# Kernel tuning notes

Measured on AMD Instinct MI355X. Metric: run time of the kernel, lower is better.

## Reference

```python
import jax, jax.numpy as jnp
import numpy as np

WINDOW_SIZE = 11
SIGMA = 1.5
WEIGHTS = np.array([0.0448, 0.2856, 0.3001, 0.2363, 0.1333], dtype=np.float32)
LEVELS = 5


def _gaussian(ws, sigma):
    x = np.arange(ws, dtype=np.float32)
    g = np.exp(-((x - ws // 2) ** 2) / (2.0 * sigma ** 2))
    return g / g.sum()


def _window3d(ws, channel):
    g = _gaussian(ws, SIGMA)
    w3 = np.einsum('i,j,k->ijk', g, g, g).astype(np.float32)  # [ws,ws,ws]
    # OIDHW, depthwise: O=channel, I=1
    return jnp.asarray(np.broadcast_to(w3[None, None], (channel, 1, ws, ws, ws)))


def _conv3d(x, w, channel):
    return jax.lax.conv_general_dilated(
        x, w, window_strides=(1, 1, 1), padding='VALID',
        dimension_numbers=('NCDHW', 'OIDHW', 'NCDHW'),
        feature_group_count=channel)


def _avg_pool3d(x):
    s = jax.lax.reduce_window(x, 0.0, jax.lax.add,
                              (1, 1, 2, 2, 2), (1, 1, 2, 2, 2), 'VALID')
    return s / 8.0


def _ssim(img1, img2, window_size):
    _, channel, d, h, w = img1.shape
    # val_range=None branch: L derived from img1 statistics
    max_val = jnp.where(jnp.max(img1) > 128, 255.0, 1.0)
    min_val = jnp.where(jnp.min(img1) < -0.5, -1.0, 0.0)
    L = max_val - min_val
    real_size = min(window_size, d, h, w)
    win = _window3d(real_size, channel)

    mu1 = _conv3d(img1, win, channel)
    mu2 = _conv3d(img2, win, channel)
    mu1_sq = mu1 * mu1
    mu2_sq = mu2 * mu2
    mu1_mu2 = mu1 * mu2
    sigma1_sq = _conv3d(img1 * img1, win, channel) - mu1_sq
    sigma2_sq = _conv3d(img2 * img2, win, channel) - mu2_sq
    sigma12 = _conv3d(img1 * img2, win, channel) - mu1_mu2

    C1 = (0.01 * L) ** 2
    C2 = (0.03 * L) ** 2
    v1 = 2.0 * sigma12 + C2
    v2 = sigma1_sq + sigma2_sq + C2
    cs = jnp.mean(v1 / v2)
    ssim_map = (2.0 * mu1_mu2 + C1) * v1 / ((mu1_sq + mu2_sq + C1) * v2)
    return jnp.mean(ssim_map), cs


def setup_inputs() -> dict:
    key = jax.random.key(0)
    k1, k2 = jax.random.split(key)
    shape = (2, 1, 192, 192, 192)
    img1 = jax.random.normal(k1, shape, dtype=jnp.float32)
    img2 = jax.random.normal(k2, shape, dtype=jnp.float32)
    return {"img1": img1, "img2": img2}


def reference(img1, img2):
    weights = jnp.asarray(WEIGHTS)
    ssims, mcs = [], []
    for _ in range(LEVELS):
        sim, cs = _ssim(img1, img2, WINDOW_SIZE)
        ssims.append(sim)
        mcs.append(cs)
        img1 = _avg_pool3d(img1)
        img2 = _avg_pool3d(img2)
    ssims = jnp.stack(ssims)
    mcs = jnp.stack(mcs)
    pow1 = mcs ** weights
    pow2 = ssims ** weights
    return jnp.prod(pow1[:-1]) * pow2[-1]
```

## Files before the change

kernel.cpp:

```cpp
#include <hip/hip_runtime.h>
#include <math.h>


__device__ __forceinline__ unsigned enc_f(float f) {
    unsigned u = __float_as_uint(f);
    return (u & 0x80000000u) ? ~u : (u | 0x80000000u);
}
__device__ __forceinline__ float dec_f(unsigned e) {
    unsigned u = (e & 0x80000000u) ? (e ^ 0x80000000u) : ~e;
    return __uint_as_float(u);
}

__global__ void init_kernel(float* wsf) {
    unsigned* wsu = (unsigned*)wsf;
    int t = threadIdx.x;
    if (t < 10)       wsf[t] = 0.0f;
    else if (t < 15)  wsu[t] = 0xFFFFFFFFu;
    else if (t < 20)  wsu[t] = 0u;
    else if (t == 20) wsu[t] = 0u;
}

struct PyrParams {
    const float* src[2];
    float* dst[2][4];
};

__launch_bounds__(256, 4)
__global__ void pyramid_kernel(PyrParams P, float* wsf) {
    __shared__ float L1[16 * 256];
    __shared__ float L2[512];
    __shared__ float L3[64];
    __shared__ float smn[4], smx[4];
    unsigned* wsu = (unsigned*)wsf;

    const int tid = threadIdx.x;
    int blk = blockIdx.x;
    int r = blk % 216; blk /= 216;
    int batch = blk & 1;
    int im = blk >> 1;
    const int rx = r % 6, ry = (r / 6) % 6, rz = r / 36;

    const long N0 = 192L * 192 * 192;
    const float* src = P.src[im] + (long)batch * N0;
    float* d1 = P.dst[im][0] + (long)batch * 96 * 96 * 96;
    float* d2 = P.dst[im][1] + (long)batch * 48 * 48 * 48;
    float* d3 = P.dst[im][2] + (long)batch * 24 * 24 * 24;
    float* d4 = P.dst[im][3] + (long)batch * 12 * 12 * 12;

    const int tx = tid & 15, ty = tid >> 4;
    float mnv[5], mxv[5];
#pragma unroll
    for (int l = 0; l < 5; l++) { mnv[l] = INFINITY; mxv[l] = -INFINITY; }

    const long D = 192, D2 = 192L * 192;
    const int gx = 2 * (rx * 16 + tx);
    const int gy = 2 * (ry * 16 + ty);
#pragma unroll 4
    for (int z = 0; z < 16; z++) {
        const int gz = 2 * (rz * 16 + z);
        long base = (long)gz * D2 + (long)gy * D + gx;
        float2 a00 = *(const float2*)(src + base);
        float2 a01 = *(const float2*)(src + base + D);
        float2 a10 = *(const float2*)(src + base + D2);
        float2 a11 = *(const float2*)(src + base + D2 + D);
        float lo = fminf(fminf(fminf(a00.x, a00.y), fminf(a01.x, a01.y)),
                         fminf(fminf(a10.x, a10.y), fminf(a11.x, a11.y)));
        float hi = fmaxf(fmaxf(fmaxf(a00.x, a00.y), fmaxf(a01.x, a01.y)),
                         fmaxf(fmaxf(a10.x, a10.y), fmaxf(a11.x, a11.y)));
        mnv[0] = fminf(mnv[0], lo); mxv[0] = fmaxf(mxv[0], hi);
        float s = (a00.x + a00.y + a01.x + a01.y +
                   a10.x + a10.y + a11.x + a11.y) * 0.125f;
        mnv[1] = fminf(mnv[1], s); mxv[1] = fmaxf(mxv[1], s);
        d1[(long)(rz * 16 + z) * 96 * 96 + (ry * 16 + ty) * 96 + (rx * 16 + tx)] = s;
        L1[z * 256 + ty * 16 + tx] = s;
    }
    __syncthreads();

#pragma unroll
    for (int k = 0; k < 2; k++) {
        int o = tid + (k << 8);
        int x = o & 7, y = (o >> 3) & 7, z = o >> 6;
        float s = (L1[(2 * z) * 256 + (2 * y) * 16 + 2 * x] +
                   L1[(2 * z) * 256 + (2 * y) * 16 + 2 * x + 1] +
                   L1[(2 * z) * 256 + (2 * y + 1) * 16 + 2 * x] +
                   L1[(2 * z) * 256 + (2 * y + 1) * 16 + 2 * x + 1] +
                   L1[(2 * z + 1) * 256 + (2 * y) * 16 + 2 * x] +
                   L1[(2 * z + 1) * 256 + (2 * y) * 16 + 2 * x + 1] +
                   L1[(2 * z + 1) * 256 + (2 * y + 1) * 16 + 2 * x] +
                   L1[(2 * z + 1) * 256 + (2 * y + 1) * 16 + 2 * x + 1]) * 0.125f;
        mnv[2] = fminf(mnv[2], s); mxv[2] = fmaxf(mxv[2], s);
        d2[(long)(rz * 8 + z) * 48 * 48 + (ry * 8 + y) * 48 + (rx * 8 + x)] = s;
        L2[o] = s;
    }
    __syncthreads();

    if (tid < 64) {
        int x = tid & 3, y = (tid >> 2) & 3, z = tid >> 4;
        float s = (L2[(2 * z) * 64 + (2 * y) * 8 + 2 * x] +
                   L2[(2 * z) * 64 + (2 * y) * 8 + 2 * x + 1] +
                   L2[(2 * z) * 64 + (2 * y + 1) * 8 + 2 * x] +
                   L2[(2 * z) * 64 + (2 * y + 1) * 8 + 2 * x + 1] +
                   L2[(2 * z + 1) * 64 + (2 * y) * 8 + 2 * x] +
                   L2[(2 * z + 1) * 64 + (2 * y) * 8 + 2 * x + 1] +
                   L2[(2 * z + 1) * 64 + (2 * y + 1) * 8 + 2 * x] +
                   L2[(2 * z + 1) * 64 + (2 * y + 1) * 8 + 2 * x + 1]) * 0.125f;
        mnv[3] = fminf(mnv[3], s); mxv[3] = fmaxf(mxv[3], s);
        d3[(long)(rz * 4 + z) * 24 * 24 + (ry * 4 + y) * 24 + (rx * 4 + x)] = s;
        L3[tid] = s;
    }
    __syncthreads();

    if (tid < 8) {
        int x = tid & 1, y = (tid >> 1) & 1, z = tid >> 2;
        float s = (L3[(2 * z) * 16 + (2 * y) * 4 + 2 * x] +
                   L3[(2 * z) * 16 + (2 * y) * 4 + 2 * x + 1] +
                   L3[(2 * z) * 16 + (2 * y + 1) * 4 + 2 * x] +
                   L3[(2 * z) * 16 + (2 * y + 1) * 4 + 2 * x + 1] +
                   L3[(2 * z + 1) * 16 + (2 * y) * 4 + 2 * x] +
                   L3[(2 * z + 1) * 16 + (2 * y) * 4 + 2 * x + 1] +
                   L3[(2 * z + 1) * 16 + (2 * y + 1) * 4 + 2 * x] +
                   L3[(2 * z + 1) * 16 + (2 * y + 1) * 4 + 2 * x + 1]) * 0.125f;
        mnv[4] = fminf(mnv[4], s); mxv[4] = fmaxf(mxv[4], s);
        d4[(long)(rz * 2 + z) * 12 * 12 + (ry * 2 + y) * 12 + (rx * 2 + x)] = s;
    }

    const int lane = tid & 63, w = tid >> 6;
#pragma unroll
    for (int l = 0; l < 5; l++) {
        float mn = mnv[l], mx = mxv[l];
        for (int o = 32; o; o >>= 1) {
            mn = fminf(mn, __shfl_down(mn, o));
            mx = fmaxf(mx, __shfl_down(mx, o));
        }
        __syncthreads();
        if (lane == 0) { smn[w] = mn; smx[w] = mx; }
        __syncthreads();
        if (tid == 0 && im == 0) {
            for (int i = 1; i < 4; i++) { mn = fminf(mn, smn[i]); mx = fmaxf(mx, smx[i]); }
            atomicMin(&wsu[10 + l], enc_f(mn));
            atomicMax(&wsu[15 + l], enc_f(mx));
        }
    }
}

#define TSX 16
#define TSY 32
#define EXR 42
#define EXC 26
#define SPS 30
#define NPIX (EXR * EXC)
#define TPS 17

struct AllParams {
    const float* A[5];
    const float* B[5];
    int D[5], O[5], zc[5], nTx[5], nTy[5];
    int blk0[6];
    float* out;
    double cnt[5];
};

__launch_bounds__(256, 2)
__attribute__((amdgpu_waves_per_eu(2, 2)))
__global__ void ssim_all_kernel(AllParams P, float* wsf) {
    __shared__ __align__(16) float2 S[EXR * SPS];
    __shared__ __align__(16) float4 TX4[EXR * TPS];
    __shared__ float TXe[EXR * TPS];
    __shared__ float2 RED[256];

    const int tid = threadIdx.x;
    const int col = tid & 15;
    const int yg  = tid >> 4;

    int level = 0;
    {
        int b = blockIdx.x;
#pragma unroll
        for (int l = 1; l < 5; l++)
            if (b >= P.blk0[l]) level = l;
    }
    int rel = blockIdx.x - P.blk0[level];
    const int D   = P.D[level];
    const int O   = P.O[level];
    const int ZC  = P.zc[level];
    const int nTx = P.nTx[level];
    const int nTy = P.nTy[level];

    const int tx = rel % nTx;  rel /= nTx;
    const int ty = rel % nTy;  rel /= nTy;
    const int batch = rel & 1;
    const int chunk = rel >> 1;

    const int oz0 = chunk * ZC;
    const int oz1 = min(oz0 + ZC, O);
    const int nplanes = oz1 - oz0 + 10;
    const int ox0 = tx * TSX;
    const int oy0 = ty * TSY;
    const int D2  = D * D;
    const float* A = P.A[level] + (long)batch * D * D2;
    const float* B = P.B[level] + (long)batch * D * D2;

    float g[11];
    {
        float s = 0.f;
#pragma unroll
        for (int i = 0; i < 11; i++) {
            float d = (float)(i - 5);
            g[i] = expf(-d * d / 4.5f);
            s += g[i];
        }
#pragma unroll
        for (int i = 0; i < 11; i++) g[i] /= s;
    }

    const unsigned* wsu = (const unsigned*)wsf;
    float mxv = dec_f(wsu[15 + level]);
    float mnv = dec_f(wsu[10 + level]);
    float maxval = (mxv > 128.f) ? 255.f : 1.f;
    float minval = (mnv < -0.5f) ? -1.f : 0.f;
    float Lr = maxval - minval;
    float C1 = 0.01f * Lr; C1 *= C1;
    float C2 = 0.03f * Lr; C2 *= C2;

    int  poff[5], sidx[5];
    bool pval[5];
#pragma unroll
    for (int k = 0; k < 5; k++) {
        int idx = tid + (k << 8);
        pval[k] = (idx < NPIX);
        int row = idx / EXC;
        int c   = idx - row * EXC;
        sidx[k] = row * SPS + c;
        int gy = min(oy0 + row, D - 1);
        int gx = min(ox0 + c,   D - 1);
        poff[k] = gy * D + gx;
    }

    float Acc[10][11] = {};
    float ssim_acc = 0.f, cs_acc = 0.f;

    const bool vx  = (ox0 + col < O);
    const bool vy0 = vx && (oy0 + 2 * yg < O);
    const bool vy1 = vx && (oy0 + 2 * yg + 1 < O);

    float2 Pld[5];
    {
        long zoff = (long)oz0 * D2;
#pragma unroll
        for (int k = 0; k < 5; k++)
            if (pval[k]) Pld[k] = make_float2(A[zoff + poff[k]], B[zoff + poff[k]]);
    }

    for (int pc = 0; pc < nplanes; ++pc) {
        __syncthreads();
#pragma unroll
        for (int k = 0; k < 5; k++)
            if (pval[k]) S[sidx[k]] = Pld[k];
        if (pc + 1 < nplanes) {
            long zoff = (long)(oz0 + pc + 1) * D2;
#pragma unroll
            for (int k = 0; k < 5; k++)
                if (pval[k]) Pld[k] = make_float2(A[zoff + poff[k]], B[zoff + poff[k]]);
        }
        __syncthreads();

        if (tid < EXR * 4) {
            int row = tid >> 2;
            int cg  = tid & 3;
            const float4* srow = (const float4*)(S + row * SPS);
            float pa[14], pb[14];
#pragma unroll
            for (int i = 0; i < 7; i++) {
                float4 q = srow[2 * cg + i];
                pa[2 * i] = q.x; pb[2 * i] = q.y;
                pa[2 * i + 1] = q.z; pb[2 * i + 1] = q.w;
            }
#pragma unroll
            for (int cc = 0; cc < 4; cc++) {
                float m1 = 0.f, m2 = 0.f, aa = 0.f, bb = 0.f, ab = 0.f;
#pragma unroll
                for (int j = 0; j < 11; j++) {
                    float w = g[j];
                    float a = pa[cc + j], b = pb[cc + j];
                    float wa = w * a, wb = w * b;
                    m1 += wa; m2 += wb;
                    aa += wa * a; bb += wb * b; ab += wa * b;
                }
                int o = row * TPS + 4 * cg + cc;
                TX4[o] = make_float4(m1, m2, aa, bb);
                TXe[o] = ab;
            }
        }
        __syncthreads();

        float se[5] = {0.f, 0.f, 0.f, 0.f, 0.f};
        float so[5] = {0.f, 0.f, 0.f, 0.f, 0.f};
#pragma unroll
        for (int j = 0; j < 12; j++) {
            int o = (2 * yg + j) * TPS + col;
            float4 q = TX4[o];
            float e  = TXe[o];
            if (j < 11) {
                float w = g[j];
                se[0] += w * q.x; se[1] += w * q.y; se[2] += w * q.z;
                se[3] += w * q.w; se[4] += w * e;
            }
            if (j > 0) {
                float w = g[j - 1];
                so[0] += w * q.x; so[1] += w * q.y; so[2] += w * q.z;
                so[3] += w * q.w; so[4] += w * e;
            }
        }

#pragma unroll
        for (int f = 0; f < 5; f++) {
#pragma unroll
            for (int k = 0; k < 10; k++)
                Acc[2 * f][k] = fmaf(g[10 - k], se[f], Acc[2 * f][k + 1]);
            Acc[2 * f][10] = g[0] * se[f];
#pragma unroll
            for (int k = 0; k < 10; k++)
                Acc[2 * f + 1][k] = fmaf(g[10 - k], so[f], Acc[2 * f + 1][k + 1]);
            Acc[2 * f + 1][10] = g[0] * so[f];
        }

        if (pc >= 10) {
#pragma unroll
            for (int r = 0; r < 2; r++) {
                bool valid = r ? vy1 : vy0;
                if (!valid) continue;
                float m1  = Acc[0 + r][0], m2  = Acc[2 + r][0];
                float s11 = Acc[4 + r][0], s22 = Acc[6 + r][0], s12 = Acc[8 + r][0];
                float mu11 = m1 * m1, mu22 = m2 * m2, mu12 = m1 * m2;
                float sg1 = s11 - mu11, sg2 = s22 - mu22, sg12 = s12 - mu12;
                float v1 = 2.f * sg12 + C2;
                float v2 = sg1 + sg2 + C2;
                cs_acc   += v1 / v2;
                ssim_acc += ((2.f * mu12 + C1) * v1) / ((mu11 + mu22 + C1) * v2);
            }
        }
    }

    RED[tid] = make_float2(ssim_acc, cs_acc);
    __syncthreads();
    for (int s = 128; s > 0; s >>= 1) {
        if (tid < s) {
            RED[tid].x += RED[tid + s].x;
            RED[tid].y += RED[tid + s].y;
        }
        __syncthreads();
    }
    if (tid == 0) {
        atomicAdd(&wsf[level],     RED[0].x);
        atomicAdd(&wsf[5 + level], RED[0].y);
        __threadfence();
        unsigned prev = atomicAdd((unsigned*)wsf + 20, 1u);
        if (prev == (unsigned)(P.blk0[5] - 1)) {
            double w[5];
            w[0] = (double)0.0448f; w[1] = (double)0.2856f; w[2] = (double)0.3001f;
            w[3] = (double)0.2363f; w[4] = (double)0.1333f;
            double prod = 1.0;
            for (int l = 0; l < 4; l++) {
                float cs = atomicAdd(&wsf[5 + l], 0.0f);
                prod *= pow((double)cs / P.cnt[l], w[l]);
            }
            float sm = atomicAdd(&wsf[4], 0.0f);
            prod *= pow((double)sm / P.cnt[4], w[4]);
            P.out[0] = (float)prod;
        }
    }
}

extern "C" void kernel_launch(void* const* d_in, const int* in_sizes, int n_in,
                              void* d_out, int out_size, void* d_ws, size_t ws_size,
                              hipStream_t stream) {
    (void)in_sizes; (void)n_in; (void)out_size; (void)ws_size;
    const float* img1 = (const float*)d_in[0];
    const float* img2 = (const float*)d_in[1];
    float* wsf = (float*)d_ws;
    float* out = (float*)d_out;

    const int Ds[5]  = {192, 96, 48, 24, 12};
    const int ZCs[5] = {26, 16, 14, 14, 2};

    float* bufA[5] = {nullptr};
    float* bufB[5] = {nullptr};
    size_t o = 32;
    for (int l = 1; l < 5; l++) {
        long n = 2L * Ds[l] * Ds[l] * Ds[l];
        bufA[l] = wsf + o; o += (size_t)n;
        bufB[l] = wsf + o; o += (size_t)n;
    }

    init_kernel<<<1, 64, 0, stream>>>(wsf);

    PyrParams PP;
    PP.src[0] = img1; PP.src[1] = img2;
    for (int l = 1; l < 5; l++) { PP.dst[0][l - 1] = bufA[l]; PP.dst[1][l - 1] = bufB[l]; }
    pyramid_kernel<<<216 * 2 * 2, 256, 0, stream>>>(PP, wsf);

    AllParams P;
    P.A[0] = img1; P.B[0] = img2;
    for (int l = 1; l < 5; l++) { P.A[l] = bufA[l]; P.B[l] = bufB[l]; }
    P.out = out;
    int acc = 0;
    for (int l = 0; l < 5; l++) {
        int D = Ds[l], O = D - 10, ZC = ZCs[l];
        int nTx = (O + TSX - 1) / TSX;
        int nTy = (O + TSY - 1) / TSY;
        int ZCn = (O + ZC - 1) / ZC;
        P.D[l] = D; P.O[l] = O; P.zc[l] = ZC; P.nTx[l] = nTx; P.nTy[l] = nTy;
        P.blk0[l] = acc;
        acc += nTx * nTy * 2 * ZCn;
        double Od = (double)O;
        P.cnt[l] = 2.0 * Od * Od * Od;
    }
    P.blk0[5] = acc;
    ssim_all_kernel<<<acc, 256, 0, stream>>>(P, wsf);
}
```

Before: 356.5 us.

## Merge a²+b² into one filtered field, double-buffer plane tile, raise occupancy

Sigma1 and sigma2 appear in the result only as a sum, so the kernel now filters a²+b² as a single field. That cuts the separable-filter state from five fields to four, shrinking the Acc registers and the transpose buffer. The input plane tile is double-buffered in shared memory, which removes one __syncthreads per plane. The launch bounds are relaxed to target 3-4 waves per EU, and the Gaussian weights are computed on the host and passed as kernel arguments. The row pass is restructured as a scatter over the loaded values. Higher occupancy risks register spills.

```diff
diff --git a/kernel.cpp b/kernel.cpp
--- a/kernel.cpp
+++ b/kernel.cpp
@@ -154,18 +154,18 @@
 struct AllParams {
     const float* A[5];
     const float* B[5];
+    float* out;
+    double cnt[5];
     int D[5], O[5], zc[5], nTx[5], nTy[5];
     int blk0[6];
-    float* out;
-    double cnt[5];
+    float g[11];
 };
 
-__launch_bounds__(256, 2)
-__attribute__((amdgpu_waves_per_eu(2, 2)))
+__launch_bounds__(256)
+__attribute__((amdgpu_waves_per_eu(3, 4)))
 __global__ void ssim_all_kernel(AllParams P, float* wsf) {
-    __shared__ __align__(16) float2 S[EXR * SPS];
+    __shared__ __align__(16) float2 S[2][EXR * SPS];
     __shared__ __align__(16) float4 TX4[EXR * TPS];
-    __shared__ float TXe[EXR * TPS];
     __shared__ float2 RED[256];
 
     const int tid = threadIdx.x;
@@ -199,19 +199,6 @@
     const int D2  = D * D;
     const float* A = P.A[level] + (long)batch * D * D2;
     const float* B = P.B[level] + (long)batch * D * D2;
-
-    float g[11];
-    {
-        float s = 0.f;
-#pragma unroll
-        for (int i = 0; i < 11; i++) {
-            float d = (float)(i - 5);
-            g[i] = expf(-d * d / 4.5f);
-            s += g[i];
-        }
-#pragma unroll
-        for (int i = 0; i < 11; i++) g[i] /= s;
-    }
 
     const unsigned* wsu = (const unsigned*)wsf;
     float mxv = dec_f(wsu[15 + level]);
@@ -236,7 +223,7 @@
         poff[k] = gy * D + gx;
     }
 
-    float Acc[10][11] = {};
+    float Acc[8][11] = {};
     float ssim_acc = 0.f, cs_acc = 0.f;
 
     const bool vx  = (ox0 + col < O);
@@ -252,10 +239,10 @@
     }
 
     for (int pc = 0; pc < nplanes; ++pc) {
-        __syncthreads();
+        float2* Sc = S[pc & 1];
 #pragma unroll
         for (int k = 0; k < 5; k++)
-            if (pval[k]) S[sidx[k]] = Pld[k];
+            if (pval[k]) Sc[sidx[k]] = Pld[k];
         if (pc + 1 < nplanes) {
             long zoff = (long)(oz0 + pc + 1) * D2;
 #pragma unroll
@@ -265,63 +252,67 @@
         __syncthreads();
 
         if (tid < EXR * 4) {
-            int row = tid >> 2;
-            int cg  = tid & 3;
-            const float4* srow = (const float4*)(S + row * SPS);
-            float pa[14], pb[14];
+            const int row = tid >> 2;
+            const int cg  = tid & 3;
+            const float4* srow = (const float4*)(Sc + row * SPS);
+            float m1[4] = {}, m2[4] = {}, sq[4] = {}, sab[4] = {};
 #pragma unroll
             for (int i = 0; i < 7; i++) {
-                float4 q = srow[2 * cg + i];
-                pa[2 * i] = q.x; pb[2 * i] = q.y;
-                pa[2 * i + 1] = q.z; pb[2 * i + 1] = q.w;
+                float4 qv = srow[2 * cg + i];
+#pragma unroll
+                for (int h = 0; h < 2; h++) {
+                    const int jj = 2 * i + h;
+                    float a = h ? qv.z : qv.x;
+                    float b = h ? qv.w : qv.y;
+                    float e  = a * b;
+                    float s2 = fmaf(a, a, b * b);
+#pragma unroll
+                    for (int cc = 0; cc < 4; cc++) {
+                        const int j = jj - cc;
+                        if (j >= 0 && j <= 10) {
+                            float w = P.g[j];
+                            m1[cc]  = fmaf(w, a,  m1[cc]);
+                            m2[cc]  = fmaf(w, b,  m2[cc]);
+                            sq[cc]  = fmaf(w, s2, sq[cc]);
+                            sab[cc] = fmaf(w, e,  sab[cc]);
+                        }
+                    }
+                }
             }
 #pragma unroll
-            for (int cc = 0; cc < 4; cc++) {
-                float m1 = 0.f, m2 = 0.f, aa = 0.f, bb = 0.f, ab = 0.f;
-#pragma unroll
-                for (int j = 0; j < 11; j++) {
-                    float w = g[j];
-                    float a = pa[cc + j], b = pb[cc + j];
-                    float wa = w * a, wb = w * b;
-                    m1 += wa; m2 += wb;
-                    aa += wa * a; bb += wb * b; ab += wa * b;
-                }
-                int o = row * TPS + 4 * cg + cc;
-                TX4[o] = make_float4(m1, m2, aa, bb);
-                TXe[o] = ab;
-            }
+            for (int cc = 0; cc < 4; cc++)
+                TX4[row * TPS + 4 * cg + cc] =
+                    make_float4(m1[cc], m2[cc], sq[cc], sab[cc]);
         }
         __syncthreads();
 
-        float se[5] = {0.f, 0.f, 0.f, 0.f, 0.f};
-        float so[5] = {0.f, 0.f, 0.f, 0.f, 0.f};
+        float se[4] = {0.f, 0.f, 0.f, 0.f};
+        float so[4] = {0.f, 0.f, 0.f, 0.f};
 #pragma unroll
         for (int j = 0; j < 12; j++) {
-            int o = (2 * yg + j) * TPS + col;
-            float4 q = TX4[o];
-            float e  = TXe[o];
+            float4 q = TX4[(2 * yg + j) * TPS + col];
             if (j < 11) {
-                float w = g[j];
-                se[0] += w * q.x; se[1] += w * q.y; se[2] += w * q.z;
-                se[3] += w * q.w; se[4] += w * e;
+                float w = P.g[j];
+                se[0] = fmaf(w, q.x, se[0]); se[1] = fmaf(w, q.y, se[1]);
+                se[2] = fmaf(w, q.z, se[2]); se[3] = fmaf(w, q.w, se[3]);
             }
             if (j > 0) {
-                float w = g[j - 1];
-                so[0] += w * q.x; so[1] += w * q.y; so[2] += w * q.z;
-                so[3] += w * q.w; so[4] += w * e;
+                float w = P.g[j - 1];
+                so[0] = fmaf(w, q.x, so[0]); so[1] = fmaf(w, q.y, so[1]);
+                so[2] = fmaf(w, q.z, so[2]); so[3] = fmaf(w, q.w, so[3]);
             }
         }
 
 #pragma unroll
-        for (int f = 0; f < 5; f++) {
+        for (int f = 0; f < 4; f++) {
 #pragma unroll
             for (int k = 0; k < 10; k++)
-                Acc[2 * f][k] = fmaf(g[10 - k], se[f], Acc[2 * f][k + 1]);
-            Acc[2 * f][10] = g[0] * se[f];
+                Acc[2 * f][k] = fmaf(P.g[10 - k], se[f], Acc[2 * f][k + 1]);
+            Acc[2 * f][10] = P.g[0] * se[f];
 #pragma unroll
             for (int k = 0; k < 10; k++)
-                Acc[2 * f + 1][k] = fmaf(g[10 - k], so[f], Acc[2 * f + 1][k + 1]);
-            Acc[2 * f + 1][10] = g[0] * so[f];
+                Acc[2 * f + 1][k] = fmaf(P.g[10 - k], so[f], Acc[2 * f + 1][k + 1]);
+            Acc[2 * f + 1][10] = P.g[0] * so[f];
         }
 
         if (pc >= 10) {
@@ -329,12 +320,13 @@
             for (int r = 0; r < 2; r++) {
                 bool valid = r ? vy1 : vy0;
                 if (!valid) continue;
-                float m1  = Acc[0 + r][0], m2  = Acc[2 + r][0];
-                float s11 = Acc[4 + r][0], s22 = Acc[6 + r][0], s12 = Acc[8 + r][0];
-                float mu11 = m1 * m1, mu22 = m2 * m2, mu12 = m1 * m2;
-                float sg1 = s11 - mu11, sg2 = s22 - mu22, sg12 = s12 - mu12;
+                float m1v = Acc[0 + r][0], m2v = Acc[2 + r][0];
+                float sqv = Acc[4 + r][0], sbv = Acc[6 + r][0];
+                float mu11 = m1v * m1v, mu22 = m2v * m2v, mu12 = m1v * m2v;
+                float sg12 = sbv - mu12;
+                float sgs  = sqv - mu11 - mu22;
                 float v1 = 2.f * sg12 + C2;
-                float v2 = sg1 + sg2 + C2;
+                float v2 = sgs + C2;
                 cs_acc   += v1 / v2;
                 ssim_acc += ((2.f * mu12 + C1) * v1) / ((mu11 + mu22 + C1) * v2);
             }
@@ -416,5 +408,16 @@
         P.cnt[l] = 2.0 * Od * Od * Od;
     }
     P.blk0[5] = acc;
+
+    {
+        float s = 0.f;
+        for (int i = 0; i < 11; i++) {
+            float d = (float)(i - 5);
+            P.g[i] = expf(-d * d / 4.5f);
+            s += P.g[i];
+        }
+        for (int i = 0; i < 11; i++) P.g[i] /= s;
+    }
+
     ssim_all_kernel<<<acc, 256, 0, stream>>>(P, wsf);
 }
```

Result: slower. 535.8 us (+50.3%).
